# Kernel optimization log

Hardware: AMD Instinct MI355X
Metric: run time of the kernel (lower is better)

Reference implementation:

```python
import jax, jax.numpy as jnp
import numpy as np

N = 10000   # num_nodes (batch=1)
E = 160000  # num edges
CIN, H, T, OUT, K = 32, 64, 12, 12, 3


def _conv1d(x, w, b, pad):
    # x: [N, C_in, T], w: [C_out, C_in, K]
    out = jax.lax.conv_general_dilated(
        x, w, window_strides=(1,), padding=[(pad, pad)],
        dimension_numbers=('NCH', 'OIH', 'NCH'))
    return out + b[None, :, None]


def _gated_tconv(x, w, b):
    # GatedTemporalConv (dropout = identity in eval)
    out = _conv1d(x, w, b, K // 2)
    P, Q = jnp.split(out, 2, axis=1)
    return P * jax.nn.sigmoid(Q)


def _gcn(x, W, b, src, dst, ew):
    # PyG GCNConv, vectorized over all T timesteps in one fused pass.
    # x: [N, C_in, T], W: [C_out, C_in]
    xt = jnp.einsum('nct,oc->not', x, W)
    loop = jnp.arange(N)
    srcl = jnp.concatenate([src, loop])
    dstl = jnp.concatenate([dst, loop])
    ewl = jnp.concatenate([ew, jnp.ones((N,), ew.dtype)])
    deg = jax.ops.segment_sum(ewl, dstl, num_segments=N)
    dis = jnp.where(deg > 0, jax.lax.rsqrt(deg), 0.0)
    norm = dis[srcl] * ewl * dis[dstl]                      # [E+N]
    msg = xt[srcl] * norm[:, None, None]                    # [E+N, C_out, T]
    out = jax.ops.segment_sum(msg, dstl, num_segments=N)    # [N, C_out, T]
    return out + b[None, :, None]


def setup_inputs() -> dict:
    key = jax.random.key(0)
    ks = jax.random.split(key, 20)
    rn = lambda k, s: jax.random.normal(k, s, jnp.float32) * 0.05
    return {
        'x': jax.random.normal(ks[0], (N, CIN, T), jnp.float32),
        'edge_index': jax.random.randint(ks[1], (2, E), 0, N),
        'edge_weight': jax.random.uniform(ks[2], (E,), jnp.float32),
        'tc1a_w': rn(ks[3], (2 * H, CIN, K)), 'tc1a_b': rn(ks[4], (2 * H,)),
        'gc1_w': rn(ks[5], (H, H)),           'gc1_b': rn(ks[6], (H,)),
        'tc1b_w': rn(ks[7], (2 * H, H, K)),   'tc1b_b': rn(ks[8], (2 * H,)),
        'tc2a_w': rn(ks[9], (2 * H, H, K)),   'tc2a_b': rn(ks[10], (2 * H,)),
        'gc2_w': rn(ks[11], (H, H)),          'gc2_b': rn(ks[12], (H,)),
        'tc2b_w': rn(ks[13], (2 * H, H, K)),  'tc2b_b': rn(ks[14], (2 * H,)),
        'fin_w': rn(ks[15], (OUT, H, T)),     'fin_b': rn(ks[16], (OUT,)),
    }


def reference(x, edge_index, edge_weight,
              tc1a_w, tc1a_b, gc1_w, gc1_b, tc1b_w, tc1b_b,
              tc2a_w, tc2a_b, gc2_w, gc2_b, tc2b_w, tc2b_b,
              fin_w, fin_b):
    src, dst = edge_index[0], edge_index[1]
    h = _gated_tconv(x, tc1a_w, tc1a_b)
    h = jax.nn.relu(_gcn(h, gc1_w, gc1_b, src, dst, edge_weight))
    h = _gated_tconv(h, tc1b_w, tc1b_b)
    h = _gated_tconv(h, tc2a_w, tc2a_b)
    h = jax.nn.relu(_gcn(h, gc2_w, gc2_b, src, dst, edge_weight))
    h = _gated_tconv(h, tc2b_w, tc2b_b)
    h = _conv1d(h, fin_w, fin_b, 0)          # [N, OUT, 1] (kernel == T)
    h = h[:, :, 0]                            # squeeze(-1)
    return h.reshape(1, N, OUT)               # batch_size = 1
```

## Files before the change

kernel.cpp:

```cpp
#include <hip/hip_runtime.h>
#include <hip/hip_bf16.h>
#include <stdint.h>

#define N_NODES 10000
#define N_EDGES 160000
#define BUCKET 128

typedef unsigned short u16;
typedef unsigned int u32;
typedef short s16v8 __attribute__((ext_vector_type(8)));
typedef float f32v4 __attribute__((ext_vector_type(4)));

__device__ __forceinline__ float bf2f(u16 v){ return __uint_as_float(((u32)v) << 16); }
__device__ __forceinline__ u16 f2bf(float f){
    u32 u = __float_as_uint(f);
    u32 r = (u + 0x7fffu + ((u >> 16) & 1u)) >> 16;
    return (u16)r;
}

struct SmallPtrs { const void* p[14]; };

__device__ __constant__ const int g_seg_off[15] = {
    0, 12288, 12416, 16512, 16576, 41152, 41280,
    65856, 65984, 70080, 70144, 94720, 94848, 104064, 104076
};
__device__ __constant__ const int g_seg_kind[14] = {
    1, 0, 0, 0, 2, 0, 2, 0, 0, 0, 2, 0, 0, 0
};

__global__ void k_convert_init(SmallPtrs ps, u16* __restrict__ dst,
                               float* deg, int* cur){
    int i = blockIdx.x * blockDim.x + threadIdx.x;
    if (i < 104076){
        int seg = 0, base = 0;
#pragma unroll
        for (int s = 0; s < 14; s++){
            if (i >= g_seg_off[s]){ seg = s; base = g_seg_off[s]; }
        }
        int li = i - base;
        float v = ((const float*)ps.p[seg])[li];
        int kind = g_seg_kind[seg];
        int dsto = li;
        if (kind){
            int CIN = (kind == 1) ? 32 : 64;
            int o = li / (3 * CIN);
            int rem = li - o * (3 * CIN);
            int c = rem / 3, d = rem - c * 3;
            dsto = d * 128 * CIN + o * CIN + c;
        }
        dst[base + dsto] = f2bf(v);
    }
    if (i < N_NODES){ deg[i] = 1.0f; cur[i] = 0; }
}

__launch_bounds__(256, 2)
__global__ void k_gconv_count(const float* __restrict__ xin, const u16* __restrict__ wg,
                              const u16* __restrict__ bg, u16* __restrict__ out,
                              const int* __restrict__ ei, const float* __restrict__ ew,
                              float* deg, int* cur, int2* __restrict__ epack){
    if (blockIdx.x >= 1250){
        int e = (blockIdx.x - 1250) * 256 + threadIdx.x;
        if (e < N_EDGES){
            int s = ei[e];
            int d = ei[N_EDGES + e];
            float wv = ew[e];
            atomicAdd(&deg[d], wv);
            int p = atomicAdd(&cur[d], 1);
            if (p < BUCKET) epack[d * BUCKET + p] = make_int2(s, __float_as_int(wv));
        }
        return;
    }
    __shared__ __attribute__((aligned(16))) u16 xT[8][14][40];
    __shared__ __attribute__((aligned(16))) u16 Ho[8][12][72];
    int tid = threadIdx.x;
    int n0 = blockIdx.x * 8;

    int lane = tid & 63, wave = tid >> 6;
    int col = lane & 15, quad = lane >> 4;
    int o_p = wave * 16 + col, o_q = o_p + 64;

    s16v8 Bf[3][2];
#pragma unroll
    for (int pq = 0; pq < 2; pq++){
        int o = pq ? o_q : o_p;
#pragma unroll
        for (int d = 0; d < 3; d++)
            Bf[d][pq] = *(const s16v8*)(wg + d * 4096 + o * 32 + quad * 8);
    }

    for (int i = tid; i < 8 * 40; i += 256){
        int g = i / 40, c = i % 40;
        xT[g][0][c] = 0; xT[g][13][c] = 0;
    }
    {
        int g = tid >> 5, c = tid & 31;
        const float4* p = (const float4*)(xin + ((size_t)(n0 + g) * 32 + c) * 12);
        float4 v0 = p[0], v1 = p[1], v2 = p[2];
        xT[g][1][c] = f2bf(v0.x);  xT[g][2][c] = f2bf(v0.y);
        xT[g][3][c] = f2bf(v0.z);  xT[g][4][c] = f2bf(v0.w);
        xT[g][5][c] = f2bf(v1.x);  xT[g][6][c] = f2bf(v1.y);
        xT[g][7][c] = f2bf(v1.z);  xT[g][8][c] = f2bf(v1.w);
        xT[g][9][c] = f2bf(v2.x);  xT[g][10][c] = f2bf(v2.y);
        xT[g][11][c] = f2bf(v2.z); xT[g][12][c] = f2bf(v2.w);
    }
    __syncthreads();

    f32v4 aP[6], aQ[6];
#pragma unroll
    for (int mt = 0; mt < 6; mt++){ aP[mt] = (f32v4)0.f; aQ[mt] = (f32v4)0.f; }
#pragma unroll
    for (int mt = 0; mt < 6; mt++){
        int m = mt * 16 + col;
        int g = m / 12, t = m - 12 * g;
#pragma unroll
        for (int d = 0; d < 3; d++){
            s16v8 a = *(const s16v8*)&xT[g][t + d][quad * 8];
            aP[mt] = __builtin_amdgcn_mfma_f32_16x16x32_bf16(a, Bf[d][0], aP[mt], 0, 0, 0);
            aQ[mt] = __builtin_amdgcn_mfma_f32_16x16x32_bf16(a, Bf[d][1], aQ[mt], 0, 0, 0);
        }
    }
    float bP = bf2f(bg[o_p]), bQ = bf2f(bg[o_q]);
#pragma unroll
    for (int mt = 0; mt < 6; mt++){
#pragma unroll
        for (int r = 0; r < 4; r++){
            int m2 = mt * 16 + quad * 4 + r;
            int g = m2 / 12, t = m2 - 12 * g;
            float pv = aP[mt][r] + bP, qv = aQ[mt][r] + bQ;
            Ho[g][t][o_p] = f2bf(pv / (1.f + __expf(-qv)));
        }
    }
    __syncthreads();
    for (int i = tid; i < 768; i += 256){
        int g = i / 96, r = i % 96, t = r / 8, ch = r % 8;
        *(s16v8*)(out + (size_t)(n0 + g) * 768 + t * 64 + ch * 8) = *(const s16v8*)&Ho[g][t][ch * 8];
    }
}

__launch_bounds__(256, 4)
__global__ void k_gather(const u16* __restrict__ src, const float* __restrict__ deg,
                         const int* __restrict__ cur, const int2* __restrict__ ep,
                         u16* __restrict__ z){
    int slice = blockIdx.x & 7;
    int nb = blockIdx.x >> 3;
    int tid = threadIdx.x;
    int nl = tid >> 5;
    int sub = tid & 31;
    int eg = sub >> 3;
    int l8 = sub & 7;
    int n = nb * 8 + nl;
    int base = slice * 96 + l8 * 12;
    float dn = rsqrtf(deg[n]);

    float acc[12];
    if (eg == 0){
        float sw = dn * dn;
        const u16* xr = src + (size_t)n * 768 + base;
#pragma unroll
        for (int k = 0; k < 3; k++){
            ushort4 v = *(const ushort4*)(xr + k * 4);
            acc[k * 4 + 0] = sw * bf2f(v.x); acc[k * 4 + 1] = sw * bf2f(v.y);
            acc[k * 4 + 2] = sw * bf2f(v.z); acc[k * 4 + 3] = sw * bf2f(v.w);
        }
    } else {
#pragma unroll
        for (int k = 0; k < 12; k++) acc[k] = 0.f;
    }

    int e = cur[n]; if (e > BUCKET) e = BUCKET;
    const int2* eb = ep + (size_t)n * BUCKET;
    int p = eg;
    for (; p + 4 < e; p += 8){
        int2 e0 = eb[p], e1 = eb[p + 4];
        float w0 = dn * __int_as_float(e0.y) * rsqrtf(deg[e0.x]);
        float w1 = dn * __int_as_float(e1.y) * rsqrtf(deg[e1.x]);
        const u16* q0 = src + (size_t)e0.x * 768 + base;
        const u16* q1 = src + (size_t)e1.x * 768 + base;
        ushort4 a0 = *(const ushort4*)(q0);
        ushort4 a1 = *(const ushort4*)(q0 + 4);
        ushort4 a2 = *(const ushort4*)(q0 + 8);
        ushort4 c0 = *(const ushort4*)(q1);
        ushort4 c1 = *(const ushort4*)(q1 + 4);
        ushort4 c2 = *(const ushort4*)(q1 + 8);
        acc[0] = fmaf(w0, bf2f(a0.x), acc[0]); acc[1] = fmaf(w0, bf2f(a0.y), acc[1]);
        acc[2] = fmaf(w0, bf2f(a0.z), acc[2]); acc[3] = fmaf(w0, bf2f(a0.w), acc[3]);
        acc[4] = fmaf(w0, bf2f(a1.x), acc[4]); acc[5] = fmaf(w0, bf2f(a1.y), acc[5]);
        acc[6] = fmaf(w0, bf2f(a1.z), acc[6]); acc[7] = fmaf(w0, bf2f(a1.w), acc[7]);
        acc[8] = fmaf(w0, bf2f(a2.x), acc[8]); acc[9] = fmaf(w0, bf2f(a2.y), acc[9]);
        acc[10] = fmaf(w0, bf2f(a2.z), acc[10]); acc[11] = fmaf(w0, bf2f(a2.w), acc[11]);
        acc[0] = fmaf(w1, bf2f(c0.x), acc[0]); acc[1] = fmaf(w1, bf2f(c0.y), acc[1]);
        acc[2] = fmaf(w1, bf2f(c0.z), acc[2]); acc[3] = fmaf(w1, bf2f(c0.w), acc[3]);
        acc[4] = fmaf(w1, bf2f(c1.x), acc[4]); acc[5] = fmaf(w1, bf2f(c1.y), acc[5]);
        acc[6] = fmaf(w1, bf2f(c1.z), acc[6]); acc[7] = fmaf(w1, bf2f(c1.w), acc[7]);
        acc[8] = fmaf(w1, bf2f(c2.x), acc[8]); acc[9] = fmaf(w1, bf2f(c2.y), acc[9]);
        acc[10] = fmaf(w1, bf2f(c2.z), acc[10]); acc[11] = fmaf(w1, bf2f(c2.w), acc[11]);
    }
    if (p < e){
        int2 e0 = eb[p];
        float w0 = dn * __int_as_float(e0.y) * rsqrtf(deg[e0.x]);
        const u16* q0 = src + (size_t)e0.x * 768 + base;
#pragma unroll
        for (int k = 0; k < 3; k++){
            ushort4 v = *(const ushort4*)(q0 + k * 4);
            acc[k * 4 + 0] = fmaf(w0, bf2f(v.x), acc[k * 4 + 0]);
            acc[k * 4 + 1] = fmaf(w0, bf2f(v.y), acc[k * 4 + 1]);
            acc[k * 4 + 2] = fmaf(w0, bf2f(v.z), acc[k * 4 + 2]);
            acc[k * 4 + 3] = fmaf(w0, bf2f(v.w), acc[k * 4 + 3]);
        }
    }
#pragma unroll
    for (int k = 0; k < 12; k++){
        acc[k] += __shfl_xor(acc[k], 8, 64);
        acc[k] += __shfl_xor(acc[k], 16, 64);
    }
    if (eg == 0){
        u16* zo = z + (size_t)n * 768 + base;
#pragma unroll
        for (int k = 0; k < 3; k++){
            ushort4 hv;
            hv.x = f2bf(acc[k * 4 + 0]); hv.y = f2bf(acc[k * 4 + 1]);
            hv.z = f2bf(acc[k * 4 + 2]); hv.w = f2bf(acc[k * 4 + 3]);
            *(ushort4*)(zo + k * 4) = hv;
        }
    }
}

#define XIDX(g, row, c) (((g) * 14 + (row)) * 72 + (c))

template<bool LAST>
__launch_bounds__(256, 4)
__global__ void k_fused(const u16* __restrict__ z,
                        const u16* __restrict__ Wmix, const u16* __restrict__ bmix,
                        const u16* __restrict__ w1, const u16* __restrict__ b1,
                        const u16* __restrict__ w2, const u16* __restrict__ b2,
                        const u16* __restrict__ fw, const u16* __restrict__ fb,
                        u16* __restrict__ outMid, float* __restrict__ outFin){
    __shared__ __attribute__((aligned(16))) u16 bufX[8 * 14 * 72];
    __shared__ __attribute__((aligned(16))) u16 bufY[8 * 14 * 72];
    int tid = threadIdx.x;
    int n0 = blockIdx.x * 8;
    int lane = tid & 63, wave = tid >> 6;
    int col = lane & 15, quad = lane >> 4;
    int o_p = wave * 16 + col, o_q = o_p + 64;

    for (int i = tid; i < 8 * 72; i += 256){
        int g = i / 72, c = i % 72;
        bufX[XIDX(g, 0, c)] = 0; bufX[XIDX(g, 13, c)] = 0;
        bufY[XIDX(g, 0, c)] = 0; bufY[XIDX(g, 13, c)] = 0;
    }
    for (int i = tid; i < 768; i += 256){
        int g = i / 96, r = i % 96, t = r >> 3, ch = r & 7;
        *(s16v8*)&bufX[XIDX(g, 1 + t, ch * 8)] =
            *(const s16v8*)(z + (size_t)(n0 + g) * 768 + t * 64 + ch * 8);
    }
    __syncthreads();

    {
        f32v4 accm[6];
#pragma unroll
        for (int mt = 0; mt < 6; mt++) accm[mt] = (f32v4)0.f;
#pragma unroll
        for (int ks = 0; ks < 2; ks++){
            s16v8 Bm = *(const s16v8*)(Wmix + (size_t)o_p * 64 + ks * 32 + quad * 8);
#pragma unroll
            for (int mt = 0; mt < 6; mt++){
                int m = mt * 16 + col;
                int g = m / 12, t = m - 12 * g;
                s16v8 a = *(const s16v8*)&bufX[XIDX(g, 1 + t, ks * 32 + quad * 8)];
                accm[mt] = __builtin_amdgcn_mfma_f32_16x16x32_bf16(a, Bm, accm[mt], 0, 0, 0);
            }
        }
        float bm = bf2f(bmix[o_p]);
#pragma unroll
        for (int mt = 0; mt < 6; mt++){
#pragma unroll
            for (int r = 0; r < 4; r++){
                int m2 = mt * 16 + quad * 4 + r;
                int g = m2 / 12, t = m2 - 12 * g;
                bufY[XIDX(g, 1 + t, o_p)] = f2bf(fmaxf(accm[mt][r] + bm, 0.f));
            }
        }
    }
    __syncthreads();

    {
        f32v4 aP[6], aQ[6];
#pragma unroll
        for (int mt = 0; mt < 6; mt++){ aP[mt] = (f32v4)0.f; aQ[mt] = (f32v4)0.f; }
#pragma unroll
        for (int ks = 0; ks < 2; ks++){
            s16v8 Bf[3][2];
#pragma unroll
            for (int pq = 0; pq < 2; pq++){
                int o = pq ? o_q : o_p;
#pragma unroll
                for (int d = 0; d < 3; d++)
                    Bf[d][pq] = *(const s16v8*)(w1 + d * 8192 + o * 64 + ks * 32 + quad * 8);
            }
#pragma unroll
            for (int mt = 0; mt < 6; mt++){
                int m = mt * 16 + col;
                int g = m / 12, t = m - 12 * g;
#pragma unroll
                for (int d = 0; d < 3; d++){
                    s16v8 a = *(const s16v8*)&bufY[XIDX(g, t + d, ks * 32 + quad * 8)];
                    aP[mt] = __builtin_amdgcn_mfma_f32_16x16x32_bf16(a, Bf[d][0], aP[mt], 0, 0, 0);
                    aQ[mt] = __builtin_amdgcn_mfma_f32_16x16x32_bf16(a, Bf[d][1], aQ[mt], 0, 0, 0);
                }
            }
        }
        float bP = bf2f(b1[o_p]), bQ = bf2f(b1[o_q]);
#pragma unroll
        for (int mt = 0; mt < 6; mt++){
#pragma unroll
            for (int r = 0; r < 4; r++){
                int m2 = mt * 16 + quad * 4 + r;
                int g = m2 / 12, t = m2 - 12 * g;
                float pv = aP[mt][r] + bP, qv = aQ[mt][r] + bQ;
                u16 hv = f2bf(pv / (1.f + __expf(-qv)));
                if (LAST) bufX[g * 1008 + o_p * 12 + t] = hv;
                else      bufX[XIDX(g, 1 + t, o_p)] = hv;
            }
        }
    }
    __syncthreads();

    if (!LAST){
        f32v4 aP[6], aQ[6];
#pragma unroll
        for (int mt = 0; mt < 6; mt++){ aP[mt] = (f32v4)0.f; aQ[mt] = (f32v4)0.f; }
#pragma unroll
        for (int ks = 0; ks < 2; ks++){
            s16v8 Bf[3][2];
#pragma unroll
            for (int pq = 0; pq < 2; pq++){
                int o = pq ? o_q : o_p;
#pragma unroll
                for (int d = 0; d < 3; d++)
                    Bf[d][pq] = *(const s16v8*)(w2 + d * 8192 + o * 64 + ks * 32 + quad * 8);
            }
#pragma unroll
            for (int mt = 0; mt < 6; mt++){
                int m = mt * 16 + col;
                int g = m / 12, t = m - 12 * g;
#pragma unroll
                for (int d = 0; d < 3; d++){
                    s16v8 a = *(const s16v8*)&bufX[XIDX(g, t + d, ks * 32 + quad * 8)];
                    aP[mt] = __builtin_amdgcn_mfma_f32_16x16x32_bf16(a, Bf[d][0], aP[mt], 0, 0, 0);
                    aQ[mt] = __builtin_amdgcn_mfma_f32_16x16x32_bf16(a, Bf[d][1], aQ[mt], 0, 0, 0);
                }
            }
        }
        float bP = bf2f(b2[o_p]), bQ = bf2f(b2[o_q]);
#pragma unroll
        for (int mt = 0; mt < 6; mt++){
#pragma unroll
            for (int r = 0; r < 4; r++){
                int m2 = mt * 16 + quad * 4 + r;
                int g = m2 / 12, t = m2 - 12 * g;
                float pv = aP[mt][r] + bP, qv = aQ[mt][r] + bQ;
                bufY[XIDX(g, 1 + t, o_p)] = f2bf(pv / (1.f + __expf(-qv)));
            }
        }
        __syncthreads();
        for (int i = tid; i < 768; i += 256){
            int g = i / 96, r = i % 96, t = r / 8, ch = r % 8;
            *(s16v8*)(outMid + (size_t)(n0 + g) * 768 + t * 64 + ch * 8) =
                *(const s16v8*)&bufY[XIDX(g, 1 + t, ch * 8)];
        }
    } else {
        if (wave == 0){
            f32v4 accF = {0.f, 0.f, 0.f, 0.f};
            int g8 = col & 7;
#pragma unroll
            for (int ks = 0; ks < 24; ks++){
                s16v8 a = *(const s16v8*)&bufX[g8 * 1008 + ks * 32 + quad * 8];
                s16v8 bfr = {0, 0, 0, 0, 0, 0, 0, 0};
                if (col < 12)
                    bfr = *(const s16v8*)(fw + (size_t)col * 768 + ks * 32 + quad * 8);
                accF = __builtin_amdgcn_mfma_f32_16x16x32_bf16(a, bfr, accF, 0, 0, 0);
            }
            if (col < 12 && quad < 2){
                float bb = bf2f(fb[col]);
#pragma unroll
                for (int r = 0; r < 4; r++){
                    int g = quad * 4 + r;
                    outFin[(size_t)(n0 + g) * 12 + col] = accF[r] + bb;
                }
            }
        }
    }
}

static inline size_t align256(size_t x){ return (x + 255) & ~(size_t)255; }

extern "C" void kernel_launch(void* const* d_in, const int* in_sizes, int n_in,
                              void* d_out, int out_size, void* d_ws, size_t ws_size,
                              hipStream_t stream){
    const float* x  = (const float*)d_in[0];
    const int* ei   = (const int*)d_in[1];
    const float* ew = (const float*)d_in[2];

    char* w = (char*)d_ws;
    u16* bufA    = (u16*)w;  w += align256((size_t)N_NODES * 768 * sizeof(u16));
    u16* bufB    = (u16*)w;  w += align256((size_t)N_NODES * 768 * sizeof(u16));
    u16* zA      = (u16*)w;  w += align256((size_t)N_NODES * 768 * sizeof(u16));
    u16* zB      = (u16*)w;  w += align256((size_t)N_NODES * 768 * sizeof(u16));
    float* deg   = (float*)w; w += align256(N_NODES * sizeof(float));
    int* cur     = (int*)w;   w += align256(N_NODES * sizeof(int));
    int2* epack  = (int2*)w;  w += align256((size_t)N_NODES * BUCKET * sizeof(int2));
    u16* cvt     = (u16*)w;   w += align256(104076 * sizeof(u16));

    u16* tc1a_w = cvt + 0;
    u16* tc1a_b = cvt + 12288;
    u16* gc1_w  = cvt + 12416;
    u16* gc1_b  = cvt + 16512;
    u16* tc1b_w = cvt + 16576;
    u16* tc1b_b = cvt + 41152;
    u16* tc2a_w = cvt + 41280;
    u16* tc2a_b = cvt + 65856;
    u16* gc2_w  = cvt + 65984;
    u16* gc2_b  = cvt + 70080;
    u16* tc2b_w = cvt + 70144;
    u16* tc2b_b = cvt + 94720;
    u16* fin_w  = cvt + 94848;
    u16* fin_b  = cvt + 104064;

    SmallPtrs ps;
    ps.p[0]  = d_in[3];  ps.p[1]  = d_in[4];
    ps.p[2]  = d_in[5];  ps.p[3]  = d_in[6];
    ps.p[4]  = d_in[7];  ps.p[5]  = d_in[8];
    ps.p[6]  = d_in[9];  ps.p[7]  = d_in[10];
    ps.p[8]  = d_in[11]; ps.p[9]  = d_in[12];
    ps.p[10] = d_in[13]; ps.p[11] = d_in[14];
    ps.p[12] = d_in[15]; ps.p[13] = d_in[16];

    k_convert_init<<<(104076 + 255) / 256, 256, 0, stream>>>(ps, cvt, deg, cur);
    k_gconv_count<<<1250 + 625, 256, 0, stream>>>(x, tc1a_w, tc1a_b, bufA, ei, ew, deg, cur, epack);

    k_gather<<<1250 * 8, 256, 0, stream>>>(bufA, deg, cur, epack, zA);
    k_fused<false><<<1250, 256, 0, stream>>>(zA, gc1_w, gc1_b, tc1b_w, tc1b_b,
                                             tc2a_w, tc2a_b, nullptr, nullptr,
                                             bufB, nullptr);
    k_gather<<<1250 * 8, 256, 0, stream>>>(bufB, deg, cur, epack, zB);
    k_fused<true><<<1250, 256, 0, stream>>>(zB, gc2_w, gc2_b, tc2b_w, tc2b_b,
                                            nullptr, nullptr, fin_w, fin_b,
                                            nullptr, (float*)d_out);
}
```

Measured before the change: 241.1 us.

## Precompute GCN edge normalization once and share LDS buffers in gconv kernel

A new k_norm kernel folds rsqrt(deg[src])*rsqrt(deg[dst]) into the packed edge weights once. Both gather passes then read a ready weight instead of doing a dependent random deg lookup and rsqrt per edge in each pass. Separately, the first conv kernel now aliases its input and output LDS tiles behind an extra barrier and raises launch bounds to 4 blocks per CU to improve occupancy. The cost is one extra kernel launch and a read-modify-write pass over the edge buckets.

After: 232.1 us. 1.04x faster.

```diff
diff --git a/kernel.cpp b/kernel.cpp
--- a/kernel.cpp
+++ b/kernel.cpp
@@ -53,7 +53,7 @@
     if (i < N_NODES){ deg[i] = 1.0f; cur[i] = 0; }
 }
 
-__launch_bounds__(256, 2)
+__launch_bounds__(256, 4)
 __global__ void k_gconv_count(const float* __restrict__ xin, const u16* __restrict__ wg,
                               const u16* __restrict__ bg, u16* __restrict__ out,
                               const int* __restrict__ ei, const float* __restrict__ ew,
@@ -70,8 +70,9 @@
         }
         return;
     }
-    __shared__ __attribute__((aligned(16))) u16 xT[8][14][40];
-    __shared__ __attribute__((aligned(16))) u16 Ho[8][12][72];
+    __shared__ __attribute__((aligned(16))) u16 shbuf[6912];
+    u16* xT = shbuf;
+    u16* Ho = shbuf;
     int tid = threadIdx.x;
     int n0 = blockIdx.x * 8;
 
@@ -90,18 +91,19 @@
 
     for (int i = tid; i < 8 * 40; i += 256){
         int g = i / 40, c = i % 40;
-        xT[g][0][c] = 0; xT[g][13][c] = 0;
+        xT[g * 560 + 0 * 40 + c] = 0; xT[g * 560 + 13 * 40 + c] = 0;
     }
     {
         int g = tid >> 5, c = tid & 31;
         const float4* p = (const float4*)(xin + ((size_t)(n0 + g) * 32 + c) * 12);
         float4 v0 = p[0], v1 = p[1], v2 = p[2];
-        xT[g][1][c] = f2bf(v0.x);  xT[g][2][c] = f2bf(v0.y);
-        xT[g][3][c] = f2bf(v0.z);  xT[g][4][c] = f2bf(v0.w);
-        xT[g][5][c] = f2bf(v1.x);  xT[g][6][c] = f2bf(v1.y);
-        xT[g][7][c] = f2bf(v1.z);  xT[g][8][c] = f2bf(v1.w);
-        xT[g][9][c] = f2bf(v2.x);  xT[g][10][c] = f2bf(v2.y);
-        xT[g][11][c] = f2bf(v2.z); xT[g][12][c] = f2bf(v2.w);
+        u16* xb = xT + g * 560 + c;
+        xb[1 * 40] = f2bf(v0.x);  xb[2 * 40] = f2bf(v0.y);
+        xb[3 * 40] = f2bf(v0.z);  xb[4 * 40] = f2bf(v0.w);
+        xb[5 * 40] = f2bf(v1.x);  xb[6 * 40] = f2bf(v1.y);
+        xb[7 * 40] = f2bf(v1.z);  xb[8 * 40] = f2bf(v1.w);
+        xb[9 * 40] = f2bf(v2.x);  xb[10 * 40] = f2bf(v2.y);
+        xb[11 * 40] = f2bf(v2.z); xb[12 * 40] = f2bf(v2.w);
     }
     __syncthreads();
 
@@ -114,11 +116,12 @@
         int g = m / 12, t = m - 12 * g;
 #pragma unroll
         for (int d = 0; d < 3; d++){
-            s16v8 a = *(const s16v8*)&xT[g][t + d][quad * 8];
+            s16v8 a = *(const s16v8*)&xT[g * 560 + (t + d) * 40 + quad * 8];
             aP[mt] = __builtin_amdgcn_mfma_f32_16x16x32_bf16(a, Bf[d][0], aP[mt], 0, 0, 0);
             aQ[mt] = __builtin_amdgcn_mfma_f32_16x16x32_bf16(a, Bf[d][1], aQ[mt], 0, 0, 0);
         }
     }
+    __syncthreads();
     float bP = bf2f(bg[o_p]), bQ = bf2f(bg[o_q]);
 #pragma unroll
     for (int mt = 0; mt < 6; mt++){
@@ -127,13 +130,27 @@
             int m2 = mt * 16 + quad * 4 + r;
             int g = m2 / 12, t = m2 - 12 * g;
             float pv = aP[mt][r] + bP, qv = aQ[mt][r] + bQ;
-            Ho[g][t][o_p] = f2bf(pv / (1.f + __expf(-qv)));
+            Ho[g * 864 + t * 72 + o_p] = f2bf(pv / (1.f + __expf(-qv)));
         }
     }
     __syncthreads();
     for (int i = tid; i < 768; i += 256){
         int g = i / 96, r = i % 96, t = r / 8, ch = r % 8;
-        *(s16v8*)(out + (size_t)(n0 + g) * 768 + t * 64 + ch * 8) = *(const s16v8*)&Ho[g][t][ch * 8];
+        *(s16v8*)(out + (size_t)(n0 + g) * 768 + t * 64 + ch * 8) =
+            *(const s16v8*)&Ho[g * 864 + t * 72 + ch * 8];
+    }
+}
+
+__global__ void k_norm(const float* __restrict__ deg, const int* __restrict__ cur,
+                       int2* __restrict__ ep){
+    int i = blockIdx.x * blockDim.x + threadIdx.x;
+    int n = i >> 7, slot = i & 127;
+    if (n >= N_NODES) return;
+    int cnt = cur[n]; if (cnt > BUCKET) cnt = BUCKET;
+    if (slot < cnt){
+        int2 e = ep[(size_t)n * BUCKET + slot];
+        float w = __int_as_float(e.y) * rsqrtf(deg[e.x]) * rsqrtf(deg[n]);
+        ep[(size_t)n * BUCKET + slot].y = __float_as_int(w);
     }
 }
 
@@ -150,11 +167,10 @@
     int l8 = sub & 7;
     int n = nb * 8 + nl;
     int base = slice * 96 + l8 * 12;
-    float dn = rsqrtf(deg[n]);
 
     float acc[12];
     if (eg == 0){
-        float sw = dn * dn;
+        float sw = 1.0f / deg[n];
         const u16* xr = src + (size_t)n * 768 + base;
 #pragma unroll
         for (int k = 0; k < 3; k++){
@@ -172,8 +188,7 @@
     int p = eg;
     for (; p + 4 < e; p += 8){
         int2 e0 = eb[p], e1 = eb[p + 4];
-        float w0 = dn * __int_as_float(e0.y) * rsqrtf(deg[e0.x]);
-        float w1 = dn * __int_as_float(e1.y) * rsqrtf(deg[e1.x]);
+        float w0 = __int_as_float(e0.y), w1 = __int_as_float(e1.y);
         const u16* q0 = src + (size_t)e0.x * 768 + base;
         const u16* q1 = src + (size_t)e1.x * 768 + base;
         ushort4 a0 = *(const ushort4*)(q0);
@@ -197,7 +212,7 @@
     }
     if (p < e){
         int2 e0 = eb[p];
-        float w0 = dn * __int_as_float(e0.y) * rsqrtf(deg[e0.x]);
+        float w0 = __int_as_float(e0.y);
         const u16* q0 = src + (size_t)e0.x * 768 + base;
 #pragma unroll
         for (int k = 0; k < 3; k++){
@@ -437,6 +452,7 @@
 
     k_convert_init<<<(104076 + 255) / 256, 256, 0, stream>>>(ps, cvt, deg, cur);
     k_gconv_count<<<1250 + 625, 256, 0, stream>>>(x, tc1a_w, tc1a_b, bufA, ei, ew, deg, cur, epack);
+    k_norm<<<(N_NODES * BUCKET) / 256, 256, 0, stream>>>(deg, cur, epack);
 
     k_gather<<<1250 * 8, 256, 0, stream>>>(bufA, deg, cur, epack, zA);
     k_fused<false><<<1250, 256, 0, stream>>>(zA, gc1_w, gc1_b, tc1b_w, tc1b_b,
```
